# Performance work log

Hardware: AMD Instinct MI355X
Metric: run time of the kernel (lower is better)

## Reference

```python
import jax, jax.numpy as jnp
import numpy as np

RCR = 5.2
RCA = 3.5
ETA_R = np.array([16.0], np.float32)                      # (1,)
SHF_R = (0.9 + 0.26875 * np.arange(16)).astype(np.float32)  # (16,)
ETA_A = np.array([8.0], np.float32)                       # (1,)
ZETA = np.array([32.0], np.float32)                       # (1,)
SHF_A = np.array([0.9, 1.55, 2.2, 2.85], np.float32)      # (4,)
SHF_Z = (np.pi / 16 + (np.pi / 8) * np.arange(8)).astype(np.float32)  # (8,)
NUM_SPECIES = 4
C, A = 16, 64
EPS = 1e-8  # torch cosine_similarity eps

# unordered species-pair index table: (s1, s2) -> triu pair id (10 pairs for 4 species)
_tbl = np.zeros((NUM_SPECIES, NUM_SPECIES), np.int32)
_k = 0
for _a in range(NUM_SPECIES):
    for _b in range(_a, NUM_SPECIES):
        _tbl[_a, _b] = _k
        _tbl[_b, _a] = _k
        _k += 1
PAIR_TABLE = jnp.asarray(_tbl)
NUM_SP_PAIRS = _k  # 10

IDX_I, IDX_J = np.triu_indices(A, k=1)  # neighbor pair combinations, P = A*(A-1)/2


def _cutoff_cosine(d, rc):
    return jnp.where(d <= rc, 0.5 * jnp.cos(np.pi * d / rc) + 0.5, 0.0)


def setup_inputs() -> dict:
    key = jax.random.key(0)
    k1, k2 = jax.random.split(key)
    species = jax.random.randint(k1, (C, A), 0, NUM_SPECIES)
    # spread atoms over a realistic box so distances span the cutoffs
    coordinates = jax.random.normal(k2, (C, A, 3), dtype=jnp.float32) * 4.0
    return {"species": species, "coordinates": coordinates}


def reference(species, coordinates):
    f32 = coordinates.dtype
    # vec[c,i,j,:] = R_i - R_j  (matches coordinates.unsqueeze(2)-unsqueeze(1))
    vec = coordinates[:, :, None, :] - coordinates[:, None, :, :]  # (C,A,A,3)
    i_idx = jnp.arange(A)
    # valid neighbor: not self, not padding (species == -1)
    valid = (i_idx[:, None] != i_idx[None, :])[None] & (species[:, None, :] != -1)  # (C,A,A)
    vec_safe = jnp.where(valid[..., None], vec, 1.0)
    d = jnp.linalg.norm(vec_safe, axis=-1)          # (C,A,A)
    d = jnp.where(valid, d, RCR + 1.0)

    # ---- radial subAEV terms: 0.25 * exp(-EtaR (d - ShfR)^2) * fc ----
    fc = _cutoff_cosine(d, RCR)                      # (C,A,A)
    shf_r = jnp.asarray(SHF_R)
    eta_r = jnp.asarray(ETA_R)[0]
    rt = 0.25 * jnp.exp(-eta_r * (d[..., None] - shf_r) ** 2) * fc[..., None]  # (C,A,A,16)
    rt = rt * valid[..., None].astype(f32)
    onehot_s = (species[:, :, None] == jnp.arange(NUM_SPECIES)).astype(f32)  # (C,A,S)
    radial_aev = jnp.einsum('cijr,cjs->cisr', rt, onehot_s)  # (C,A,S,16)
    radial_aev = radial_aev.reshape(C, A, NUM_SPECIES * SHF_R.size)

    # ---- angular subAEV terms over neighbor pairs ----
    v1 = vec[:, :, IDX_I, :]                         # (C,A,P,3)
    v2 = vec[:, :, IDX_J, :]
    pair_valid = valid[:, :, IDX_I] & valid[:, :, IDX_J]  # (C,A,P)
    v1s = jnp.where(pair_valid[..., None], v1, 1.0)
    v2s = jnp.where(pair_valid[..., None], v2, 1.0)
    d1 = jnp.linalg.norm(v1s, axis=-1)
    d2 = jnp.linalg.norm(v2s, axis=-1)
    d1 = jnp.where(pair_valid, d1, RCA + 1.0)
    d2 = jnp.where(pair_valid, d2, RCA + 1.0)
    cos_ang = 0.95 * jnp.sum(v1s * v2s, -1) / (jnp.maximum(d1, EPS) * jnp.maximum(d2, EPS))
    angles = jnp.arccos(cos_ang)                     # |cos|<=0.95 so safe
    fcj1 = _cutoff_cosine(d1, RCA)
    fcj2 = _cutoff_cosine(d2, RCA)
    # broadcast layout (..., EtaA=1, Zeta=1, ShfA=4, ShfZ=8) -> flatten to 32
    shf_a = jnp.asarray(SHF_A).reshape(1, 1, 4, 1)
    shf_z = jnp.asarray(SHF_Z).reshape(1, 1, 1, 8)
    zeta = jnp.asarray(ZETA)[0]
    eta_a = jnp.asarray(ETA_A)[0]
    ang = angles[..., None, None, None, None]        # (C,A,P,1,1,1,1)
    dm = ((d1 + d2) / 2)[..., None, None, None, None]
    factor1 = ((1 + jnp.cos(ang - shf_z)) / 2) ** zeta
    factor2 = jnp.exp(-eta_a * (dm - shf_a) ** 2)
    at = 2 * factor1 * factor2 * fcj1[..., None, None, None, None] * fcj2[..., None, None, None, None]
    P = IDX_I.size
    at = at.reshape(C, A, P, 32) * pair_valid[..., None].astype(f32)  # (C,A,P,32)

    # species-pair one-hot over the P neighbor pairs
    sp1 = jnp.clip(species[:, IDX_I], 0, NUM_SPECIES - 1)  # (C,P); padding masked by pair_valid
    sp2 = jnp.clip(species[:, IDX_J], 0, NUM_SPECIES - 1)
    pid = PAIR_TABLE[sp1, sp2]                       # (C,P)
    onehot_p = (pid[..., None] == jnp.arange(NUM_SP_PAIRS)).astype(f32)  # (C,P,10)
    angular_aev = jnp.einsum('cipz,cpt->citz', at, onehot_p)  # (C,A,10,32)
    angular_aev = angular_aev.reshape(C, A, NUM_SP_PAIRS * 32)

    return jnp.concatenate([radial_aev, angular_aev], axis=-1)  # (C,A,384)
```

## Files before the change

### kernel.cpp

```cpp
#include <hip/hip_runtime.h>

#define RCR 5.2f
#define RCA 3.5f
#define PI_F 3.14159265358979323846f

__global__ __launch_bounds__(64)
void aev_kernel(const int* __restrict__ species,
                const float* __restrict__ coords,
                float* __restrict__ out)
{
    const int blk = blockIdx.x;
    const int c   = blk >> 6;
    const int i   = blk & 63;
    const int l   = threadIdx.x;

    const int gbase = (c * 64 + l) * 3;
    float x = coords[gbase + 0];
    float y = coords[gbase + 1];
    float z = coords[gbase + 2];
    int  sp = species[c * 64 + l];

    float xi = __shfl(x, i);
    float yi = __shfl(y, i);
    float zi = __shfl(z, i);

    float rx = xi - x, ry = yi - y, rz = zi - z;
    float d  = sqrtf(rx * rx + ry * ry + rz * rz);
    bool valid  = (l != i) && (sp != -1);
    bool rvalid = valid && (d <= RCR);
    bool avalid = valid && (d <= RCA);

    __shared__ float cx[64], cy[64], cz[64], cd_[64], cinv[64], cfa[64];
    __shared__ int   csp[64];
    __shared__ float rd[64], rfc[64];
    __shared__ int   rsp[64];
    __shared__ int   pairab[1953];
    __shared__ float acc[320];

    for (int t = l; t < 320; t += 64) acc[t] = 0.f;

    unsigned long long rmask = __ballot(rvalid);
    unsigned long long amask = __ballot(avalid);
    const int nr = __popcll(rmask);
    const int n  = __popcll(amask);
    const unsigned long long below = (l == 0) ? 0ull : (~0ull >> (64 - l));

    if (rvalid) {
        int pos = __popcll(rmask & below);
        rd[pos]  = d;
        rfc[pos] = 0.5f * __cosf(PI_F * d * (1.0f / RCR)) + 0.5f;
        rsp[pos] = sp;
    }
    if (avalid) {
        int pos = __popcll(amask & below);
        cx[pos] = rx; cy[pos] = ry; cz[pos] = rz;
        cd_[pos]  = d;
        cinv[pos] = 1.0f / fmaxf(d, 1e-8f);
        cfa[pos]  = 0.5f * __cosf(PI_F * d * (1.0f / RCA)) + 0.5f;
        csp[pos]  = sp;
    }
    if (l < n) {
        int a = l;
        int base = a * (n - 1) - (a * (a - 1)) / 2;
        for (int b = a + 1; b < n; ++b)
            pairab[base + (b - a - 1)] = (a << 6) | b;
    }
    __syncthreads();

    const int   s   = l >> 4;
    const float shf = 0.9f + 0.26875f * (float)(l & 15);
    float racc = 0.f;
    for (int m = 0; m < nr; ++m) {
        float dd   = rd[m] - shf;
        float term = 0.25f * __expf(-16.f * dd * dd) * rfc[m];
        racc += (rsp[m] == s) ? term : 0.f;
    }

    const int   sub  = l & 31;
    const float shfa = 0.9f + 0.65f * (float)(sub >> 3);
    const float shfz = PI_F / 16.f + (PI_F / 8.f) * (float)(sub & 7);
    const float czv  = __cosf(shfz);
    const float szv  = __sinf(shfz);
    const int   np   = (n * (n - 1)) >> 1;
    const int   half = l >> 5;
    for (int p0 = 0; p0 < np; p0 += 2) {
        int p = p0 + half;
        if (p < np) {
            int ab = pairab[p];
            int a = ab >> 6, b = ab & 63;
            float dot = cx[a] * cx[b] + cy[a] * cy[b] + cz[a] * cz[b];
            float ca  = 0.95f * dot * cinv[a] * cinv[b];
            float sa  = sqrtf(fmaxf(0.f, 1.f - ca * ca));
            float dm  = 0.5f * (cd_[a] + cd_[b]);
            float fprod = 2.f * cfa[a] * cfa[b];
            int s1 = csp[a], s2 = csp[b];
            int mn = min(s1, s2), mx = max(s1, s2);
            int pid = ((mn * (7 - mn)) >> 1) + mx;
            float cdz = ca * czv + sa * szv;
            float t = 0.5f + 0.5f * cdz;
            t = t * t; t = t * t; t = t * t; t = t * t; t = t * t;
            float u = dm - shfa;
            float val = t * __expf(-8.f * u * u) * fprod;
            atomicAdd(&acc[pid * 32 + sub], val);
        }
    }
    __syncthreads();

    const long ob = (long)blk * 384;
    out[ob + l] = racc;
    #pragma unroll
    for (int t = 0; t < 5; ++t)
        out[ob + 64 + t * 64 + l] = acc[t * 64 + l];
}

extern "C" void kernel_launch(void* const* d_in, const int* in_sizes, int n_in,
                              void* d_out, int out_size, void* d_ws, size_t ws_size,
                              hipStream_t stream) {
    const int* species  = (const int*)d_in[0];
    const float* coords = (const float*)d_in[1];
    float* out          = (float*)d_out;
    aev_kernel<<<dim3(16 * 64), dim3(64), 0, stream>>>(species, coords, out);
}
```

Before: 65.78 us.

## Use four wavefronts per block and pack neighbor data into float4 LDS

Each block now runs 256 threads, so four wavefronts split the radial loop, the angular pair loop and pair-table construction, with radial partials combined through LDS atomics. Per-neighbor data is packed into float4 arrays, so each neighbor needs fewer LDS loads. The pair index for the next iteration is prefetched before the current one is computed. This targets the long serial pair loop that a single wavefront had to walk per atom. The cost is redundant coordinate loads and shuffles in every wavefront, plus more LDS atomic contention on the shared accumulator.

```diff
diff --git a/kernel.cpp b/kernel.cpp
--- a/kernel.cpp
+++ b/kernel.cpp
@@ -4,7 +4,7 @@
 #define RCA 3.5f
 #define PI_F 3.14159265358979323846f
 
-__global__ __launch_bounds__(64)
+__global__ __launch_bounds__(256)
 void aev_kernel(const int* __restrict__ species,
                 const float* __restrict__ coords,
                 float* __restrict__ out)
@@ -12,7 +12,9 @@
     const int blk = blockIdx.x;
     const int c   = blk >> 6;
     const int i   = blk & 63;
-    const int l   = threadIdx.x;
+    const int tid = threadIdx.x;
+    const int l   = tid & 63;
+    const int w   = tid >> 6;
 
     const int gbase = (c * 64 + l) * 3;
     float x = coords[gbase + 0];
@@ -30,51 +32,54 @@
     bool rvalid = valid && (d <= RCR);
     bool avalid = valid && (d <= RCA);
 
-    __shared__ float cx[64], cy[64], cz[64], cd_[64], cinv[64], cfa[64];
-    __shared__ int   csp[64];
-    __shared__ float rd[64], rfc[64];
-    __shared__ int   rsp[64];
-    __shared__ int   pairab[1953];
-    __shared__ float acc[320];
+    __shared__ float4 ang0[64];
+    __shared__ float4 ang1[64];
+    __shared__ float4 radf[64];
+    __shared__ int    pairab[1953];
+    __shared__ float  acc[320];
+    __shared__ float  raccs[64];
 
-    for (int t = l; t < 320; t += 64) acc[t] = 0.f;
+    for (int t = tid; t < 320; t += 256) acc[t] = 0.f;
+    if (tid < 64) raccs[tid] = 0.f;
 
     unsigned long long rmask = __ballot(rvalid);
     unsigned long long amask = __ballot(avalid);
     const int nr = __popcll(rmask);
     const int n  = __popcll(amask);
-    const unsigned long long below = (l == 0) ? 0ull : (~0ull >> (64 - l));
 
-    if (rvalid) {
-        int pos = __popcll(rmask & below);
-        rd[pos]  = d;
-        rfc[pos] = 0.5f * __cosf(PI_F * d * (1.0f / RCR)) + 0.5f;
-        rsp[pos] = sp;
-    }
-    if (avalid) {
-        int pos = __popcll(amask & below);
-        cx[pos] = rx; cy[pos] = ry; cz[pos] = rz;
-        cd_[pos]  = d;
-        cinv[pos] = 1.0f / fmaxf(d, 1e-8f);
-        cfa[pos]  = 0.5f * __cosf(PI_F * d * (1.0f / RCA)) + 0.5f;
-        csp[pos]  = sp;
+    if (w == 0) {
+        const unsigned long long below = (l == 0) ? 0ull : (~0ull >> (64 - l));
+        if (rvalid) {
+            int pos = __popcll(rmask & below);
+            radf[pos] = make_float4(d,
+                                    0.5f * __cosf(PI_F * d * (1.0f / RCR)) + 0.5f,
+                                    __int_as_float(sp), 0.f);
+        }
+        if (avalid) {
+            int pos = __popcll(amask & below);
+            ang0[pos] = make_float4(rx, ry, rz, d);
+            ang1[pos] = make_float4(1.0f / fmaxf(d, 1e-8f),
+                                    0.5f * __cosf(PI_F * d * (1.0f / RCA)) + 0.5f,
+                                    __int_as_float(sp), 0.f);
+        }
     }
     if (l < n) {
-        int a = l;
-        int base = a * (n - 1) - (a * (a - 1)) / 2;
-        for (int b = a + 1; b < n; ++b)
-            pairab[base + (b - a - 1)] = (a << 6) | b;
+        const int base = l * (n - 1) - (l * (l - 1)) / 2;
+        for (int b = l + 1 + w; b < n; b += 4)
+            pairab[base + (b - l - 1)] = (l << 6) | b;
     }
     __syncthreads();
 
     const int   s   = l >> 4;
     const float shf = 0.9f + 0.26875f * (float)(l & 15);
     float racc = 0.f;
-    for (int m = 0; m < nr; ++m) {
-        float dd   = rd[m] - shf;
-        float term = 0.25f * __expf(-16.f * dd * dd) * rfc[m];
-        racc += (rsp[m] == s) ? term : 0.f;
+    for (int m = w; m < nr; m += 4) {
+        float4 rv  = radf[m];
+        float  dd  = rv.x - shf;
+        float  term = 0.25f * __expf(-16.f * dd * dd) * rv.y;
+        racc += (__float_as_int(rv.z) == s) ? term : 0.f;
     }
+    atomicAdd(&raccs[l], racc);
 
     const int   sub  = l & 31;
     const float shfa = 0.9f + 0.65f * (float)(sub >> 3);
@@ -83,17 +88,25 @@
     const float szv  = __sinf(shfz);
     const int   np   = (n * (n - 1)) >> 1;
     const int   half = l >> 5;
-    for (int p0 = 0; p0 < np; p0 += 2) {
-        int p = p0 + half;
-        if (p < np) {
-            int ab = pairab[p];
-            int a = ab >> 6, b = ab & 63;
-            float dot = cx[a] * cx[b] + cy[a] * cy[b] + cz[a] * cz[b];
-            float ca  = 0.95f * dot * cinv[a] * cinv[b];
+
+    int p0_first = w * 2;
+    int p_pf = p0_first + half;
+    int ab   = (p_pf < np) ? pairab[p_pf] : 0;
+    for (int p0 = p0_first; p0 < np; p0 += 8) {
+        const int pc   = p0 + half;
+        const int ab_c = ab;
+        const int pn   = p0 + 8 + half;
+        if (pn < np) ab = pairab[pn];
+        if (pc < np) {
+            const int a = ab_c >> 6, b = ab_c & 63;
+            float4 A0 = ang0[a], A1 = ang1[a];
+            float4 B0 = ang0[b], B1 = ang1[b];
+            float dot = A0.x * B0.x + A0.y * B0.y + A0.z * B0.z;
+            float ca  = 0.95f * dot * A1.x * B1.x;
             float sa  = sqrtf(fmaxf(0.f, 1.f - ca * ca));
-            float dm  = 0.5f * (cd_[a] + cd_[b]);
-            float fprod = 2.f * cfa[a] * cfa[b];
-            int s1 = csp[a], s2 = csp[b];
+            float dm  = 0.5f * (A0.w + B0.w);
+            float fprod = 2.f * A1.y * B1.y;
+            int s1 = __float_as_int(A1.z), s2 = __float_as_int(B1.z);
             int mn = min(s1, s2), mx = max(s1, s2);
             int pid = ((mn * (7 - mn)) >> 1) + mx;
             float cdz = ca * czv + sa * szv;
@@ -107,10 +120,8 @@
     __syncthreads();
 
     const long ob = (long)blk * 384;
-    out[ob + l] = racc;
-    #pragma unroll
-    for (int t = 0; t < 5; ++t)
-        out[ob + 64 + t * 64 + l] = acc[t * 64 + l];
+    if (tid < 64) out[ob + tid] = raccs[tid];
+    for (int t = tid; t < 320; t += 256) out[ob + 64 + t] = acc[t];
 }
 
 extern "C" void kernel_launch(void* const* d_in, const int* in_sizes, int n_in,
@@ -119,5 +130,5 @@
     const int* species  = (const int*)d_in[0];
     const float* coords = (const float*)d_in[1];
     float* out          = (float*)d_out;
-    aev_kernel<<<dim3(16 * 64), dim3(64), 0, stream>>>(species, coords, out);
+    aev_kernel<<<dim3(16 * 64), dim3(256), 0, stream>>>(species, coords, out);
 }
```

After: 62.49 us. 1.05x faster.
